# Optimization experiments

Measured on AMD Instinct MI355X. Metric: run time of the kernel, lower is better.

The kernel has to match this reference:

```python
import jax, jax.numpy as jnp
import numpy as np

B, C, N, D, H, NC = 128, 9, 2048, 192, 384, 18  # batch, in_chans, time, embed, mlp_hidden, classes


def setup_inputs() -> dict:
    key = jax.random.key(0)
    ks = jax.random.split(key, 18)
    rn = lambda k, sh, s=0.02: jax.random.normal(k, sh, dtype=jnp.float32) * s
    return {
        "x": jax.random.normal(ks[0], (B, C, N), dtype=jnp.float32),
        "conv_w": rn(ks[1], (D, C, 3)),
        "conv_b": jnp.zeros((D,), jnp.float32),
        "pos_embed": jnp.zeros((1, N, D), jnp.float32),
        "qkv_w": rn(ks[2], (3 * D, D)),
        "qkv_b": jnp.zeros((3 * D,), jnp.float32),
        "proj_w": rn(ks[3], (D, D)),
        "proj_b": jnp.zeros((D,), jnp.float32),
        "ln1_g": jnp.ones((D,), jnp.float32),
        "ln1_b": jnp.zeros((D,), jnp.float32),
        "mlp_w1": rn(ks[4], (H, D)),
        "mlp_b1": jnp.zeros((H,), jnp.float32),
        "mlp_w2": rn(ks[5], (D, H)),
        "mlp_b2": jnp.zeros((D,), jnp.float32),
        "ln2_g": jnp.ones((D,), jnp.float32),
        "ln2_b": jnp.zeros((D,), jnp.float32),
        "head_w": rn(ks[6], (NC, D)),
        "head_b": jnp.zeros((NC,), jnp.float32),
    }


def _ln(x, g, b, eps=1e-5):
    m = x.mean(-1, keepdims=True)
    v = ((x - m) ** 2).mean(-1, keepdims=True)
    return (x - m) * jax.lax.rsqrt(v + eps) * g + b


def reference(x, conv_w, conv_b, pos_embed, qkv_w, qkv_b, proj_w, proj_b,
              ln1_g, ln1_b, mlp_w1, mlp_b1, mlp_w2, mlp_b2, ln2_g, ln2_b,
              head_w, head_b):
    # patch embed: Conv1d(C->D, k=3, pad=1), then [B, N, D]
    h = jax.lax.conv_general_dilated(
        x, conv_w, window_strides=(1,), padding=[(1, 1)],
        dimension_numbers=("NCH", "OIH", "NCH")) + conv_b[None, :, None]
    h = jnp.transpose(h, (0, 2, 1)) + pos_embed  # [B, N, D]

    # linear (Performer-style) attention with ReLU feature maps
    hn = _ln(h, ln1_g, ln1_b)
    qkv = hn @ qkv_w.T + qkv_b  # [B, N, 3D]
    q, k, v = jnp.split(qkv, 3, axis=-1)
    q = jax.nn.relu(q)
    k = jax.nn.relu(k)
    kv = jnp.einsum("bnd,bne->bde", k, v)       # [B, D, D]
    num = jnp.einsum("bnd,bde->bne", q, kv)      # [B, N, D]
    # NOTE: original sums q over BOTH token and feature dims -> scalar per batch
    denom = q.sum(axis=(1, 2))[:, None, None]
    attn = num / (denom + 1e-6)
    h = h + attn @ proj_w.T + proj_b

    # MLP block (exact GELU, as torch nn.GELU default)
    hn2 = _ln(h, ln2_g, ln2_b)
    m = jax.nn.gelu(hn2 @ mlp_w1.T + mlp_b1, approximate=False)
    h = h + m @ mlp_w2.T + mlp_b2

    # head: AdaptiveAvgPool1d(1) over time, then Linear
    pooled = h.mean(axis=1)  # [B, D]
    return pooled @ head_w.T + head_b  # [B, NC]
```

## Files before the change

kernel.cpp:

```cpp
#include <hip/hip_runtime.h>
#include <cmath>

#define B_   128
#define C_   9
#define N_   2048
#define D_   192
#define H_   384
#define NC_  18

typedef unsigned short ushort_t;
typedef __attribute__((ext_vector_type(8))) __bf16 bf16x8;
typedef __attribute__((ext_vector_type(8))) short short8;
typedef __attribute__((ext_vector_type(16))) float f32x16;

__device__ __forceinline__ ushort_t f2bf(float x) {
    unsigned u = __float_as_uint(x);
    return (ushort_t)((u + 0x7fffu + ((u >> 16) & 1u)) >> 16);
}
__device__ __forceinline__ float bf2f(ushort_t h) {
    return __uint_as_float(((unsigned)h) << 16);
}
__device__ __forceinline__ bf16x8 ldfrag(const ushort_t* p) {
    short8 s = *(const short8*)p;
    return __builtin_bit_cast(bf16x8, s);
}

__global__ __launch_bounds__(192) void conv_ln_k(
    const float* __restrict__ x, const float* __restrict__ w,
    const float* __restrict__ cb, const float* __restrict__ pos,
    const float* __restrict__ lng, const float* __restrict__ lnb,
    float* __restrict__ h, ushort_t* __restrict__ oh, ushort_t* __restrict__ ol)
{
    const int n0 = blockIdx.x * 64;
    const int b  = blockIdx.y;
    const int d  = threadIdx.x;

    __shared__ float xs[C_][66];
    __shared__ float tile[64][193];
    __shared__ float ps[64][3], pq[64][3];
    __shared__ float mm[64], rr[64];

    for (int e = threadIdx.x; e < C_ * 66; e += 192) {
        int c = e / 66, i = e % 66;
        int n = n0 - 1 + i;
        xs[c][i] = (n >= 0 && n < N_) ? x[((size_t)b * C_ + c) * N_ + n] : 0.f;
    }
    float wr[C_][3];
#pragma unroll
    for (int c = 0; c < C_; ++c)
#pragma unroll
        for (int t = 0; t < 3; ++t) wr[c][t] = w[(d * C_ + c) * 3 + t];
    const float bias = cb[d];
    __syncthreads();

    for (int i = 0; i < 64; ++i) {
        float acc = bias + pos[(size_t)(n0 + i) * D_ + d];
#pragma unroll
        for (int c = 0; c < C_; ++c)
#pragma unroll
            for (int t = 0; t < 3; ++t) acc += xs[c][i + t] * wr[c][t];
        tile[i][d] = acc;
    }
    __syncthreads();

    {
        int row = threadIdx.x & 63, part = threadIdx.x >> 6;
        float s = 0.f, q = 0.f;
        const float* tr = &tile[row][part * 64];
#pragma unroll 8
        for (int j = 0; j < 64; ++j) { float v = tr[j]; s += v; q += v * v; }
        ps[row][part] = s; pq[row][part] = q;
    }
    __syncthreads();
    if (threadIdx.x < 64) {
        int r = threadIdx.x;
        float s = ps[r][0] + ps[r][1] + ps[r][2];
        float q = pq[r][0] + pq[r][1] + pq[r][2];
        float m = s * (1.f / D_);
        mm[r] = m;
        rr[r] = rsqrtf(q * (1.f / D_) - m * m + 1e-5f);
    }
    __syncthreads();
    {
        const float gd = lng[d], bd = lnb[d];
        for (int i = 0; i < 64; ++i) {
            float v = tile[i][d];
            size_t idx = ((size_t)b * N_ + n0 + i) * D_ + d;
            h[idx] = v;
            float nv = (v - mm[i]) * rr[i] * gd + bd;
            ushort_t hb = f2bf(nv);
            oh[idx] = hb;
            ol[idx] = f2bf(nv - bf2f(hb));
        }
    }
}

__global__ __launch_bounds__(256) void splitw_pack_k(
    const float* __restrict__ w, ushort_t* __restrict__ hi, ushort_t* __restrict__ lo,
    int NW, int K)
{
    int i = blockIdx.x * 256 + threadIdx.x;
    if (i >= NW * K) return;
    int row = i / K, k = i % K;
    int g = row / 192, c = row % 192;
    float v = w[i];
    ushort_t hb = f2bf(v);
    size_t o = (size_t)g * K * 192 + (size_t)(k >> 4) * 3072 + (size_t)c * 16 + (k & 15);
    hi[o] = hb;
    lo[o] = f2bf(v - bf2f(hb));
}

template <int EPI, int KT, int NBY>
__global__ __launch_bounds__(256) void mgemm(
    const ushort_t* __restrict__ Ah, const ushort_t* __restrict__ Al,
    const ushort_t* __restrict__ Wh, const ushort_t* __restrict__ Wl,
    const float* __restrict__ bias, float* __restrict__ dsum,
    const float* __restrict__ lng, const float* __restrict__ lnb,
    ushort_t* __restrict__ oh, ushort_t* __restrict__ ol,
    ushort_t* __restrict__ kTh, ushort_t* __restrict__ kTl,
    ushort_t* __restrict__ vTh, ushort_t* __restrict__ vTl,
    float* __restrict__ facc)
{
    extern __shared__ ushort_t smem[];
    constexpr int NS  = KT / 16;
    constexpr int APL = 12288;

    const int tid  = threadIdx.x;
    const int lane = tid & 63;
    const int l5   = lane >> 5;
    const int wid  = tid >> 6;
    const int wr = wid >> 1, wc = wid & 1;

    int bx, by;
    {
        int gmx = gridDim.x / NBY;
        int xx = blockIdx.x & 7, ii = blockIdx.x >> 3;
        by = ii % NBY;
        bx = xx * (gmx >> 3) + ii / NBY;
    }
    const int m0 = bx * 64;
    const int batch = m0 >> 11;

    size_t wbase = 0;
    if (EPI == 0 || EPI == 1) wbase = (size_t)by * 192 * KT;
    else if (EPI == 3) wbase = (size_t)batch * D_ * D_;
    const ushort_t* Whp = Wh + wbase;
    const ushort_t* Wlp = Wl + wbase;

    auto stageChunk = [&](int kr) {
#pragma unroll
        for (int i = 0; i < 12; ++i) {
            int c = wid + i * 4;
            int plane = c & 1, k8 = c >> 1;
            const ushort_t* ap = plane ? Al : Ah;
            const ushort_t* src = ap + (size_t)(m0 + lane) * KT + kr * 192 + k8 * 8;
            __builtin_amdgcn_global_load_lds(
                (const __attribute__((address_space(1))) void*)src,
                (__attribute__((address_space(3))) void*)(smem + plane * APL + k8 * 512),
                16, 0, 0);
        }
    };

    const int wcol = (wc * 96 + (lane & 31)) * 16 + l5 * 8;
    auto loadW = [&](int sg, bf16x8* w) {
#pragma unroll
        for (int tn = 0; tn < 3; ++tn) {
            size_t off = (size_t)sg * 3072 + wcol + tn * 512;
            w[tn * 2 + 0] = ldfrag(Whp + off);
            w[tn * 2 + 1] = ldfrag(Wlp + off);
        }
    };

    f32x16 acc[3] = {};
    const int arow = (wr * 32 + (lane & 31)) * 8;

    bf16x8 w0[6], w1[6], w2[6];
    loadW(0, w0);
    if (NS > 1) loadW(1, w1);
    if (NS > 2) loadW(2, w2);

#pragma unroll
    for (int s = 0; s < NS; ++s) {
        if ((s % 12) == 0) {
            if (s) __syncthreads();
            stageChunk(s / 12);
            __syncthreads();
        }
        bf16x8* wcur = (s % 3 == 0) ? w0 : ((s % 3 == 1) ? w1 : w2);
        int ao = ((s % 12) * 2 + l5) * 512 + arow;
        bf16x8 ah = ldfrag(smem + ao);
        bf16x8 al = ldfrag(smem + APL + ao);
#pragma unroll
        for (int tn = 0; tn < 3; ++tn) {
            acc[tn] = __builtin_amdgcn_mfma_f32_32x32x16_bf16(ah, wcur[tn * 2 + 0], acc[tn], 0, 0, 0);
            acc[tn] = __builtin_amdgcn_mfma_f32_32x32x16_bf16(ah, wcur[tn * 2 + 1], acc[tn], 0, 0, 0);
            acc[tn] = __builtin_amdgcn_mfma_f32_32x32x16_bf16(al, wcur[tn * 2 + 0], acc[tn], 0, 0, 0);
        }
        if (s + 3 < NS) loadW(s + 3, wcur);
    }

    const int cb = wc * 96 + (lane & 31);
    const int rb0 = m0 + wr * 32 + 4 * l5;
    const int rl0 = wr * 32 + 4 * l5;

    if (EPI == 0) {
        if (by == 0) {
            float qsum = 0.f;
#pragma unroll
            for (int tn = 0; tn < 3; ++tn) {
                const int col = cb + tn * 32;
                const float bv = bias[col];
#pragma unroll
                for (int r = 0; r < 16; ++r) {
                    int row = rb0 + (r & 3) + 8 * (r >> 2);
                    float v = fmaxf(acc[tn][r] + bv, 0.f);
                    qsum += v;
                    ushort_t hb = f2bf(v);
                    oh[(size_t)row * D_ + col] = hb;
                    ol[(size_t)row * D_ + col] = f2bf(v - bf2f(hb));
                }
            }
            __syncthreads();
            float* red = (float*)smem;
            red[tid] = qsum;
            __syncthreads();
            for (int o = 128; o > 0; o >>= 1) {
                if (tid < o) red[tid] += red[tid + o];
                __syncthreads();
            }
            if (tid == 0) dsum[batch * 32 + ((m0 >> 6) & 31)] = red[0];
        } else {
            ushort_t* dsth = (by == 1) ? kTh : vTh;
            ushort_t* dstl = (by == 1) ? kTl : vTl;
            constexpr int STR = 72;
#pragma unroll
            for (int plane = 0; plane < 2; ++plane) {
                __syncthreads();
#pragma unroll
                for (int tn = 0; tn < 3; ++tn) {
                    const int col = cb + tn * 32;
                    const float bv = bias[by * 192 + col];
#pragma unroll
                    for (int r = 0; r < 16; ++r) {
                        int rowl = rl0 + (r & 3) + 8 * (r >> 2);
                        float v = acc[tn][r] + bv;
                        if (by == 1) v = fmaxf(v, 0.f);
                        ushort_t hb = f2bf(v);
                        smem[col * STR + rowl] = plane ? f2bf(v - bf2f(hb)) : hb;
                    }
                }
                __syncthreads();
                if (tid < 192) {
                    ushort_t* dst = plane ? dstl : dsth;
                    size_t gbase = ((size_t)batch * 192 + tid) * (size_t)N_ + (m0 & 2047);
#pragma unroll
                    for (int i2 = 0; i2 < 8; ++i2)
                        *(uint4*)(dst + gbase + i2 * 8) = *(const uint4*)&smem[tid * STR + i2 * 8];
                }
            }
        }
    } else if (EPI == 1) {
#pragma unroll
        for (int tn = 0; tn < 3; ++tn) {
            const int colg = by * 192 + cb + tn * 32;
            const float bv = bias[colg];
#pragma unroll
            for (int r = 0; r < 16; ++r) {
                int row = rb0 + (r & 3) + 8 * (r >> 2);
                float v = acc[tn][r] + bv;
                float gv = 0.5f * v * (1.f + erff(v * 0.70710678118654752f));
                ushort_t hb = f2bf(gv);
                oh[(size_t)row * H_ + colg] = hb;
                ol[(size_t)row * H_ + colg] = f2bf(gv - bf2f(hb));
            }
        }
    } else if (EPI == 2) {
        float tsum[3] = {0.f, 0.f, 0.f};
#pragma unroll
        for (int tn = 0; tn < 3; ++tn) {
            const int col = cb + tn * 32;
            const float bv = bias[col];
#pragma unroll
            for (int r = 0; r < 16; ++r) {
                int row = rb0 + (r & 3) + 8 * (r >> 2);
                float v = facc[(size_t)row * D_ + col] + acc[tn][r] + bv;
                facc[(size_t)row * D_ + col] = v;
                tsum[tn] += v;
            }
        }
#pragma unroll
        for (int tn = 0; tn < 3; ++tn) {
            float t = tsum[tn];
            t += __shfl_xor(t, 32);
            if (l5 == 0) atomicAdd(&dsum[(size_t)batch * D_ + cb + tn * 32], t);
        }
    } else if (EPI == 3) {
        float ds = 0.f;
        const float* dp = dsum + batch * 32;
#pragma unroll
        for (int j = 0; j < 32; ++j) ds += dp[j];
        const float s = 1.f / (ds + 1e-6f);
#pragma unroll
        for (int tn = 0; tn < 3; ++tn) {
            const int col = cb + tn * 32;
            const float bv = bias[col];
#pragma unroll
            for (int r = 0; r < 16; ++r) {
                int row = rb0 + (r & 3) + 8 * (r >> 2);
                float v = facc[(size_t)row * D_ + col] + acc[tn][r] * s + bv;
                facc[(size_t)row * D_ + col] = v;
                acc[tn][r] = v;
            }
        }
        __syncthreads();
        float* ls = (float*)smem;
        float* lq = ls + 128;
        float* lm = lq + 128;
        float* lr = lm + 64;
#pragma unroll
        for (int r = 0; r < 16; ++r) {
            float pv = acc[0][r] + acc[1][r] + acc[2][r];
            float qv = acc[0][r] * acc[0][r] + acc[1][r] * acc[1][r] + acc[2][r] * acc[2][r];
#pragma unroll
            for (int off = 1; off <= 16; off <<= 1) {
                pv += __shfl_xor(pv, off);
                qv += __shfl_xor(qv, off);
            }
            if ((lane & 31) == 0) {
                int rl = rl0 + (r & 3) + 8 * (r >> 2);
                ls[rl * 2 + wc] = pv;
                lq[rl * 2 + wc] = qv;
            }
        }
        __syncthreads();
        if (tid < 64) {
            float sv = ls[tid * 2] + ls[tid * 2 + 1];
            float qv = lq[tid * 2] + lq[tid * 2 + 1];
            float mv = sv * (1.f / D_);
            lm[tid] = mv;
            lr[tid] = rsqrtf(qv * (1.f / D_) - mv * mv + 1e-5f);
        }
        __syncthreads();
#pragma unroll
        for (int tn = 0; tn < 3; ++tn) {
            const int col = cb + tn * 32;
            const float gv = lng[col], bv2 = lnb[col];
#pragma unroll
            for (int r = 0; r < 16; ++r) {
                int rl = rl0 + (r & 3) + 8 * (r >> 2);
                float nv = (acc[tn][r] - lm[rl]) * lr[rl] * gv + bv2;
                ushort_t hb = f2bf(nv);
                size_t idx = (size_t)(m0 + rl) * D_ + col;
                oh[idx] = hb;
                ol[idx] = f2bf(nv - bf2f(hb));
            }
        }
    }
}

__global__ __launch_bounds__(256) void mgemm_kv(
    const ushort_t* __restrict__ Ah, const ushort_t* __restrict__ Al,
    const ushort_t* __restrict__ Wh, const ushort_t* __restrict__ Wl,
    float* __restrict__ facc, size_t span)
{
    extern __shared__ ushort_t smem[];
    constexpr int BM = 64;
    constexpr int APL = BM * 32, AK = BM * 8, AELEMS = BM * 64;
    constexpr int BUFE = AELEMS + 12288;
    constexpr int ACH = 8, NCH = ACH + 24;

    const int tid  = threadIdx.x;
    const int lane = tid & 63;
    const int l5   = lane >> 5;
    const int wid  = tid >> 6;
    const int wr = wid >> 1, wc = wid & 1;
    const int bx = blockIdx.x;
    const int m0 = bx * BM;

    const size_t wbase = (size_t)(bx / 3) * 192 * (size_t)N_;
    const ushort_t* Whp = Wh + wbase;
    const ushort_t* Wlp = Wl + wbase;

    const int seg = N_ / gridDim.z;
    const int kbeg = blockIdx.z * seg, kend = kbeg + seg;

    auto stage = [&](int buf, int k0) {
        const int base = buf * BUFE;
#pragma unroll
        for (int i = 0; i < NCH / 4; ++i) {
            int c = wid + i * 4;
            const ushort_t* src;
            int dst;
            if (c < ACH) {
                int koct = c & 3, tt = c >> 2;
                int plane = tt & 1;
                const ushort_t* ap = plane ? Al : Ah;
                src = ap + (size_t)(m0 + lane) * N_ + k0 + koct * 8;
                dst = plane * APL + koct * AK;
            } else {
                int c2 = c - ACH;
                int koct = c2 & 3, tt = c2 >> 2;
                int plane = tt & 1, rb = tt >> 1;
                const ushort_t* wp = plane ? Wlp : Whp;
                src = wp + (size_t)(rb * 64 + lane) * N_ + k0 + koct * 8;
                dst = AELEMS + plane * 6144 + koct * 1536 + rb * 512;
            }
            __builtin_amdgcn_global_load_lds(
                (const __attribute__((address_space(1))) void*)src,
                (__attribute__((address_space(3))) void*)(smem + base + dst),
                16, 0, 0);
        }
    };

    f32x16 acc[3] = {};

    const int nt = (kend - kbeg) / 32;
    stage(0, kbeg);
    __syncthreads();
    int cur = 0;
    for (int t = 0; t < nt; ++t) {
        if (t + 1 < nt) stage(cur ^ 1, kbeg + (t + 1) * 32);
        const ushort_t* bb = smem + cur * BUFE;
#pragma unroll
        for (int kh = 0; kh < 2; ++kh) {
            int ao = (kh * 2 + l5) * AK + (wr * 32 + (lane & 31)) * 8;
            bf16x8 ah = ldfrag(bb + ao);
            bf16x8 al = ldfrag(bb + APL + ao);
#pragma unroll
            for (int tn = 0; tn < 3; ++tn) {
                int wo = AELEMS + (kh * 2 + l5) * 1536 + (wc * 96 + tn * 32 + (lane & 31)) * 8;
                bf16x8 wh = ldfrag(bb + wo);
                bf16x8 wl = ldfrag(bb + wo + 6144);
                acc[tn] = __builtin_amdgcn_mfma_f32_32x32x16_bf16(ah, wh, acc[tn], 0, 0, 0);
                acc[tn] = __builtin_amdgcn_mfma_f32_32x32x16_bf16(ah, wl, acc[tn], 0, 0, 0);
                acc[tn] = __builtin_amdgcn_mfma_f32_32x32x16_bf16(al, wh, acc[tn], 0, 0, 0);
            }
        }
        __syncthreads();
        cur ^= 1;
    }

    float* fz = facc + (size_t)blockIdx.z * span;
    const int cb = wc * 96 + (lane & 31);
    const int rb0 = m0 + wr * 32 + 4 * l5;
#pragma unroll
    for (int tn = 0; tn < 3; ++tn) {
        const int col = cb + tn * 32;
#pragma unroll
        for (int r = 0; r < 16; ++r) {
            int row = rb0 + (r & 3) + 8 * (r >> 2);
            fz[(size_t)row * D_ + col] = acc[tn][r];
        }
    }
}

__global__ __launch_bounds__(256) void kv2_k(
    const float* __restrict__ pw, const float* __restrict__ kvs, size_t span,
    ushort_t* __restrict__ oh, ushort_t* __restrict__ ol)
{
    __shared__ float As[16][68];
    __shared__ float Ws[16][68];
    const int tid = threadIdx.x;
    const int tx = tid & 15, ty = tid >> 4;
    const int m0 = blockIdx.x * 64;
    const int n0 = blockIdx.y * 64;
    const int b = blockIdx.z;
    const int lm = tid >> 2;
    const int lk = (tid & 3) * 4;

    float acc[4][4] = {};
    for (int k0 = 0; k0 < D_; k0 += 16) {
        float4 av = *(const float4*)(pw + (size_t)(m0 + lm) * D_ + k0 + lk);
        As[lk + 0][lm] = av.x; As[lk + 1][lm] = av.y;
        As[lk + 2][lm] = av.z; As[lk + 3][lm] = av.w;
        const float* base = kvs + (size_t)b * D_ * D_ + (size_t)(n0 + lm) * D_ + k0 + lk;
        float4 wv = {0.f, 0.f, 0.f, 0.f};
#pragma unroll
        for (int z = 0; z < 8; ++z) {
            float4 t = *(const float4*)(base + z * span);
            wv.x += t.x; wv.y += t.y; wv.z += t.z; wv.w += t.w;
        }
        Ws[lk + 0][lm] = wv.x; Ws[lk + 1][lm] = wv.y;
        Ws[lk + 2][lm] = wv.z; Ws[lk + 3][lm] = wv.w;
        __syncthreads();
#pragma unroll
        for (int kk = 0; kk < 16; ++kk) {
            float4 a4 = *(const float4*)&As[kk][ty * 4];
            float4 w4 = *(const float4*)&Ws[kk][tx * 4];
            float a[4] = {a4.x, a4.y, a4.z, a4.w};
            float w[4] = {w4.x, w4.y, w4.z, w4.w};
#pragma unroll
            for (int i = 0; i < 4; ++i)
#pragma unroll
                for (int j = 0; j < 4; ++j) acc[i][j] += a[i] * w[j];
        }
        __syncthreads();
    }
    const int d0 = n0 + tx * 4;
#pragma unroll
    for (int i = 0; i < 4; ++i) {
        ushort_t hb[4], lb[4];
#pragma unroll
        for (int j = 0; j < 4; ++j) {
            float v = acc[i][j];
            hb[j] = f2bf(v);
            lb[j] = f2bf(v - bf2f(hb[j]));
        }
        const int e = m0 + ty * 4 + i;
        size_t off = (size_t)b * D_ * D_ + ((size_t)(d0 >> 4) * 192 + e) * 16 + (d0 & 15);
        *(uint2*)&oh[off] = make_uint2((unsigned)hb[0] | ((unsigned)hb[1] << 16),
                                       (unsigned)hb[2] | ((unsigned)hb[3] << 16));
        *(uint2*)&ol[off] = make_uint2((unsigned)lb[0] | ((unsigned)lb[1] << 16),
                                       (unsigned)lb[2] | ((unsigned)lb[3] << 16));
    }
}

__global__ __launch_bounds__(192) void head_k(
    const float* __restrict__ pooled, const float* __restrict__ hw,
    const float* __restrict__ hb, float* __restrict__ out)
{
    const int b = blockIdx.x, d = threadIdx.x;
    __shared__ float p[D_];
    p[d] = pooled[(size_t)b * D_ + d] * (1.f / N_);
    __syncthreads();
    if (d < NC_) {
        float acc = hb[d];
        for (int e = 0; e < D_; ++e) acc += p[e] * hw[d * D_ + e];
        out[b * NC_ + d] = acc;
    }
}

extern "C" void kernel_launch(void* const* d_in, const int* in_sizes, int n_in,
                              void* d_out, int out_size, void* d_ws, size_t ws_size,
                              hipStream_t stream) {
    (void)in_sizes; (void)n_in; (void)out_size;

    const float* x      = (const float*)d_in[0];
    const float* conv_w = (const float*)d_in[1];
    const float* conv_b = (const float*)d_in[2];
    const float* pos    = (const float*)d_in[3];
    const float* qkv_w  = (const float*)d_in[4];
    const float* qkv_b  = (const float*)d_in[5];
    const float* proj_w = (const float*)d_in[6];
    const float* proj_b = (const float*)d_in[7];
    const float* ln1_g  = (const float*)d_in[8];
    const float* ln1_b  = (const float*)d_in[9];
    const float* mlp_w1 = (const float*)d_in[10];
    const float* mlp_b1 = (const float*)d_in[11];
    const float* mlp_w2 = (const float*)d_in[12];
    const float* mlp_b2 = (const float*)d_in[13];
    const float* ln2_g  = (const float*)d_in[14];
    const float* ln2_b  = (const float*)d_in[15];
    const float* head_w = (const float*)d_in[16];
    const float* head_b = (const float*)d_in[17];
    float* out = (float*)d_out;

    const size_t perB =
        (size_t)N_ * D_ * 4 +
        (size_t)N_ * D_ * 2 * 2 +
        (size_t)N_ * D_ * 2 * 2 +
        (size_t)N_ * D_ * 2 * 4 +
        (size_t)D_ * D_ * 2 * 2 +
        16384;
    const size_t fixedW = 2ull * (576 * 192 + 384 * 192 + 192 * 384) * 2 + 65536;
    int BC = B_;
    while (BC > 1 && fixedW + (size_t)BC * perB > ws_size) BC >>= 1;
    const int nchunks = B_ / BC;
    const size_t rows = (size_t)BC * N_;

    char* p = (char*)d_ws;
    auto alloc = [&](size_t bytes) -> char* {
        char* r = p;
        p += (bytes + 255) & ~(size_t)255;
        return r;
    };
    ushort_t* qw_hi = (ushort_t*)alloc(576 * 192 * 2);
    ushort_t* qw_lo = (ushort_t*)alloc(576 * 192 * 2);
    ushort_t* w1_hi = (ushort_t*)alloc(384 * 192 * 2);
    ushort_t* w1_lo = (ushort_t*)alloc(384 * 192 * 2);
    ushort_t* w2_hi = (ushort_t*)alloc(192 * 384 * 2);
    ushort_t* w2_lo = (ushort_t*)alloc(192 * 384 * 2);

    const size_t szPl = rows * D_ * 2;
    float*    h      = (float*)alloc(rows * D_ * 4);
    ushort_t* hn_hi  = (ushort_t*)alloc(szPl);
    ushort_t* hn_lo  = (ushort_t*)alloc(szPl);
    ushort_t* q_hi   = (ushort_t*)alloc(szPl);
    ushort_t* q_lo   = (ushort_t*)alloc(szPl);
    ushort_t* kT_hi  = (ushort_t*)alloc(szPl);
    ushort_t* kT_lo  = (ushort_t*)alloc(szPl);
    ushort_t* vT_hi  = (ushort_t*)alloc(szPl);
    ushort_t* vT_lo  = (ushort_t*)alloc(szPl);
    ushort_t* kv2t_h = (ushort_t*)alloc((size_t)BC * D_ * D_ * 2);
    ushort_t* kv2t_l = (ushort_t*)alloc((size_t)BC * D_ * D_ * 2);
    float*    dsum   = (float*)alloc((size_t)BC * 32 * 4);
    float*    pooled = (float*)alloc((size_t)BC * D_ * 4);
    ushort_t* m_hi   = kT_hi;
    ushort_t* m_lo   = vT_hi;
    float*    kvs    = (float*)hn_hi;
    const size_t kvspan = (size_t)BC * D_ * D_;

    splitw_pack_k<<<(576 * 192 + 255) / 256, 256, 0, stream>>>(qkv_w, qw_hi, qw_lo, 576, 192);
    splitw_pack_k<<<(384 * 192 + 255) / 256, 256, 0, stream>>>(mlp_w1, w1_hi, w1_lo, 384, 192);
    splitw_pack_k<<<(192 * 384 + 255) / 256, 256, 0, stream>>>(mlp_w2, w2_hi, w2_lo, 192, 384);

    const int gm = (int)(rows / 64);
    const size_t SHA = 49152;
    const size_t SH4 = (size_t)(64 * 64 + 12288) * 2 * 2;

    for (int ch = 0; ch < nchunks; ++ch) {
        const int b0 = ch * BC;
        const float* xc = x + (size_t)b0 * C_ * N_;

        hipMemsetAsync(pooled, 0, (size_t)BC * D_ * 4, stream);

        conv_ln_k<<<dim3(N_ / 64, BC), 192, 0, stream>>>(
            xc, conv_w, conv_b, pos, ln1_g, ln1_b, h, hn_hi, hn_lo);
        mgemm<0, 192, 3><<<gm * 3, 256, SHA, stream>>>(
            hn_hi, hn_lo, qw_hi, qw_lo, qkv_b, dsum, nullptr, nullptr,
            q_hi, q_lo, kT_hi, kT_lo, vT_hi, vT_lo, nullptr);
        mgemm_kv<<<dim3(BC * 3, 1, 8), 256, SH4, stream>>>(
            kT_hi, kT_lo, vT_hi, vT_lo, kvs, kvspan);
        kv2_k<<<dim3(3, 3, BC), 256, 0, stream>>>(proj_w, kvs, kvspan, kv2t_h, kv2t_l);
        mgemm<3, 192, 1><<<gm, 256, SHA, stream>>>(
            q_hi, q_lo, kv2t_h, kv2t_l, proj_b, dsum, ln2_g, ln2_b,
            hn_hi, hn_lo, nullptr, nullptr, nullptr, nullptr, h);
        mgemm<1, 192, 2><<<gm * 2, 256, SHA, stream>>>(
            hn_hi, hn_lo, w1_hi, w1_lo, mlp_b1, nullptr, nullptr, nullptr,
            m_hi, m_lo, nullptr, nullptr, nullptr, nullptr, nullptr);
        mgemm<2, 384, 1><<<gm, 256, SHA, stream>>>(
            m_hi, m_lo, w2_hi, w2_lo, mlp_b2, pooled, nullptr, nullptr,
            nullptr, nullptr, nullptr, nullptr, nullptr, nullptr, h);
        head_k<<<BC, 192, 0, stream>>>(pooled, head_w, head_b, out + (size_t)b0 * NC_);
    }
}
```

Before: 1.575 ms.

## Fuse MLP up/down GEMMs into one kernel and stage epilogue stores via LDS

```diff
diff --git a/kernel.cpp b/kernel.cpp
--- a/kernel.cpp
+++ b/kernel.cpp
@@ -142,7 +142,7 @@
     const int batch = m0 >> 11;
 
     size_t wbase = 0;
-    if (EPI == 0 || EPI == 1) wbase = (size_t)by * 192 * KT;
+    if (EPI == 0) wbase = (size_t)by * 192 * KT;
     else if (EPI == 3) wbase = (size_t)batch * D_ * D_;
     const ushort_t* Whp = Wh + wbase;
     const ushort_t* Wlp = Wl + wbase;
@@ -206,22 +206,32 @@
     if (EPI == 0) {
         if (by == 0) {
             float qsum = 0.f;
+            __syncthreads();
 #pragma unroll
             for (int tn = 0; tn < 3; ++tn) {
                 const int col = cb + tn * 32;
                 const float bv = bias[col];
 #pragma unroll
                 for (int r = 0; r < 16; ++r) {
-                    int row = rb0 + (r & 3) + 8 * (r >> 2);
+                    int rowl = rl0 + (r & 3) + 8 * (r >> 2);
                     float v = fmaxf(acc[tn][r] + bv, 0.f);
                     qsum += v;
                     ushort_t hb = f2bf(v);
-                    oh[(size_t)row * D_ + col] = hb;
-                    ol[(size_t)row * D_ + col] = f2bf(v - bf2f(hb));
+                    smem[rowl * 192 + col] = hb;
+                    smem[APL + rowl * 192 + col] = f2bf(v - bf2f(hb));
                 }
             }
             __syncthreads();
-            float* red = (float*)smem;
+            {
+                size_t gb = (size_t)m0 * 192;
+#pragma unroll
+                for (int j = 0; j < 6; ++j) {
+                    int idx = (tid * 6 + j) * 8;
+                    *(uint4*)(oh + gb + idx) = *(const uint4*)&smem[idx];
+                    *(uint4*)(ol + gb + idx) = *(const uint4*)&smem[APL + idx];
+                }
+            }
+            float* red = (float*)(smem + 2 * APL);
             red[tid] = qsum;
             __syncthreads();
             for (int o = 128; o > 0; o >>= 1) {
@@ -259,41 +269,6 @@
                 }
             }
         }
-    } else if (EPI == 1) {
-#pragma unroll
-        for (int tn = 0; tn < 3; ++tn) {
-            const int colg = by * 192 + cb + tn * 32;
-            const float bv = bias[colg];
-#pragma unroll
-            for (int r = 0; r < 16; ++r) {
-                int row = rb0 + (r & 3) + 8 * (r >> 2);
-                float v = acc[tn][r] + bv;
-                float gv = 0.5f * v * (1.f + erff(v * 0.70710678118654752f));
-                ushort_t hb = f2bf(gv);
-                oh[(size_t)row * H_ + colg] = hb;
-                ol[(size_t)row * H_ + colg] = f2bf(gv - bf2f(hb));
-            }
-        }
-    } else if (EPI == 2) {
-        float tsum[3] = {0.f, 0.f, 0.f};
-#pragma unroll
-        for (int tn = 0; tn < 3; ++tn) {
-            const int col = cb + tn * 32;
-            const float bv = bias[col];
-#pragma unroll
-            for (int r = 0; r < 16; ++r) {
-                int row = rb0 + (r & 3) + 8 * (r >> 2);
-                float v = facc[(size_t)row * D_ + col] + acc[tn][r] + bv;
-                facc[(size_t)row * D_ + col] = v;
-                tsum[tn] += v;
-            }
-        }
-#pragma unroll
-        for (int tn = 0; tn < 3; ++tn) {
-            float t = tsum[tn];
-            t += __shfl_xor(t, 32);
-            if (l5 == 0) atomicAdd(&dsum[(size_t)batch * D_ + cb + tn * 32], t);
-        }
     } else if (EPI == 3) {
         float ds = 0.f;
         const float* dp = dsum + batch * 32;
@@ -313,7 +288,7 @@
             }
         }
         __syncthreads();
-        float* ls = (float*)smem;
+        float* ls = (float*)(smem + 2 * APL);
         float* lq = ls + 128;
         float* lm = lq + 128;
         float* lr = lm + 64;
@@ -350,11 +325,154 @@
                 int rl = rl0 + (r & 3) + 8 * (r >> 2);
                 float nv = (acc[tn][r] - lm[rl]) * lr[rl] * gv + bv2;
                 ushort_t hb = f2bf(nv);
-                size_t idx = (size_t)(m0 + rl) * D_ + col;
-                oh[idx] = hb;
-                ol[idx] = f2bf(nv - bf2f(hb));
-            }
-        }
+                smem[rl * 192 + col] = hb;
+                smem[APL + rl * 192 + col] = f2bf(nv - bf2f(hb));
+            }
+        }
+        __syncthreads();
+        {
+            size_t gb = (size_t)m0 * 192;
+#pragma unroll
+            for (int j = 0; j < 6; ++j) {
+                int idx = (tid * 6 + j) * 8;
+                *(uint4*)(oh + gb + idx) = *(const uint4*)&smem[idx];
+                *(uint4*)(ol + gb + idx) = *(const uint4*)&smem[APL + idx];
+            }
+        }
+    }
+}
+
+__global__ __launch_bounds__(256) void fused_mlp(
+    const ushort_t* __restrict__ Ah, const ushort_t* __restrict__ Al,
+    const ushort_t* __restrict__ W1h, const ushort_t* __restrict__ W1l,
+    const ushort_t* __restrict__ W2h, const ushort_t* __restrict__ W2l,
+    const float* __restrict__ b1, const float* __restrict__ b2,
+    float* __restrict__ h, float* __restrict__ pooled)
+{
+    extern __shared__ ushort_t smem[];
+    constexpr int APL = 12288;
+
+    const int tid  = threadIdx.x;
+    const int lane = tid & 63;
+    const int l5   = lane >> 5;
+    const int wid  = tid >> 6;
+    const int wr = wid >> 1, wc = wid & 1;
+
+    int bx;
+    { int xx = blockIdx.x & 7, ii = blockIdx.x >> 3; bx = xx * (gridDim.x >> 3) + ii; }
+    const int m0 = bx * 64;
+    const int batch = m0 >> 11;
+
+#pragma unroll
+    for (int i = 0; i < 12; ++i) {
+        int c = wid + i * 4;
+        int plane = c & 1, k8 = c >> 1;
+        const ushort_t* ap = plane ? Al : Ah;
+        const ushort_t* src = ap + (size_t)(m0 + lane) * 192 + k8 * 8;
+        __builtin_amdgcn_global_load_lds(
+            (const __attribute__((address_space(1))) void*)src,
+            (__attribute__((address_space(3))) void*)(smem + plane * APL + k8 * 512),
+            16, 0, 0);
+    }
+    __syncthreads();
+
+    const int wcol = (wc * 96 + (lane & 31)) * 16 + l5 * 8;
+    const int arow = (wr * 32 + (lane & 31)) * 8;
+
+    auto loadWf = [&](const ushort_t* Wh, const ushort_t* Wl, int sg, bf16x8* w) {
+#pragma unroll
+        for (int tn = 0; tn < 3; ++tn) {
+            size_t off = (size_t)sg * 3072 + wcol + tn * 512;
+            w[tn * 2 + 0] = ldfrag(Wh + off);
+            w[tn * 2 + 1] = ldfrag(Wl + off);
+        }
+    };
+
+    f32x16 accm[2][3] = {};
+#pragma unroll
+    for (int g = 0; g < 2; ++g) {
+        const ushort_t* Wh = W1h + g * 36864;
+        const ushort_t* Wl = W1l + g * 36864;
+        bf16x8 w0[6], w1[6], w2[6];
+        loadWf(Wh, Wl, 0, w0);
+        loadWf(Wh, Wl, 1, w1);
+        loadWf(Wh, Wl, 2, w2);
+#pragma unroll
+        for (int s = 0; s < 12; ++s) {
+            bf16x8* wcur = (s % 3 == 0) ? w0 : ((s % 3 == 1) ? w1 : w2);
+            int ao = (s * 2 + l5) * 512 + arow;
+            bf16x8 ah = ldfrag(smem + ao);
+            bf16x8 al = ldfrag(smem + APL + ao);
+#pragma unroll
+            for (int tn = 0; tn < 3; ++tn) {
+                accm[g][tn] = __builtin_amdgcn_mfma_f32_32x32x16_bf16(ah, wcur[tn * 2 + 0], accm[g][tn], 0, 0, 0);
+                accm[g][tn] = __builtin_amdgcn_mfma_f32_32x32x16_bf16(ah, wcur[tn * 2 + 1], accm[g][tn], 0, 0, 0);
+                accm[g][tn] = __builtin_amdgcn_mfma_f32_32x32x16_bf16(al, wcur[tn * 2 + 0], accm[g][tn], 0, 0, 0);
+            }
+            if (s + 3 < 12) loadWf(Wh, Wl, s + 3, wcur);
+        }
+    }
+
+    f32x16 acco[3] = {};
+#pragma unroll
+    for (int g = 0; g < 2; ++g) {
+        __syncthreads();
+#pragma unroll
+        for (int tn = 0; tn < 3; ++tn) {
+            const int cl = wc * 96 + tn * 32 + (lane & 31);
+            const float bv = b1[g * 192 + cl];
+#pragma unroll
+            for (int r = 0; r < 16; ++r) {
+                int rowl = wr * 32 + 4 * l5 + (r & 3) + 8 * (r >> 2);
+                float v = accm[g][tn][r] + bv;
+                float gv = 0.5f * v * (1.f + erff(v * 0.70710678118654752f));
+                ushort_t hb = f2bf(gv);
+                int ad = ((cl >> 3) * 64 + rowl) * 8 + (cl & 7);
+                smem[ad] = hb;
+                smem[APL + ad] = f2bf(gv - bf2f(hb));
+            }
+        }
+        __syncthreads();
+        bf16x8 w0[6], w1[6], w2[6];
+        loadWf(W2h, W2l, g * 12 + 0, w0);
+        loadWf(W2h, W2l, g * 12 + 1, w1);
+        loadWf(W2h, W2l, g * 12 + 2, w2);
+#pragma unroll
+        for (int s = 0; s < 12; ++s) {
+            bf16x8* wcur = (s % 3 == 0) ? w0 : ((s % 3 == 1) ? w1 : w2);
+            int ao = (s * 2 + l5) * 512 + arow;
+            bf16x8 ah = ldfrag(smem + ao);
+            bf16x8 al = ldfrag(smem + APL + ao);
+#pragma unroll
+            for (int tn = 0; tn < 3; ++tn) {
+                acco[tn] = __builtin_amdgcn_mfma_f32_32x32x16_bf16(ah, wcur[tn * 2 + 0], acco[tn], 0, 0, 0);
+                acco[tn] = __builtin_amdgcn_mfma_f32_32x32x16_bf16(ah, wcur[tn * 2 + 1], acco[tn], 0, 0, 0);
+                acco[tn] = __builtin_amdgcn_mfma_f32_32x32x16_bf16(al, wcur[tn * 2 + 0], acco[tn], 0, 0, 0);
+            }
+            if (s + 3 < 12) loadWf(W2h, W2l, g * 12 + s + 3, wcur);
+        }
+    }
+
+    const int cb = wc * 96 + (lane & 31);
+    const int rb0 = m0 + wr * 32 + 4 * l5;
+    float tsum[3] = {0.f, 0.f, 0.f};
+#pragma unroll
+    for (int tn = 0; tn < 3; ++tn) {
+        const int col = cb + tn * 32;
+        const float bv = b2[col];
+#pragma unroll
+        for (int r = 0; r < 16; ++r) {
+            int row = rb0 + (r & 3) + 8 * (r >> 2);
+            float v = h[(size_t)row * D_ + col] + acco[tn][r] + bv;
+            h[(size_t)row * D_ + col] = v;
+            tsum[tn] += v;
+        }
+    }
+#pragma unroll
+    for (int tn = 0; tn < 3; ++tn) {
+        float t = tsum[tn];
+        t += __shfl_xor(t, 32);
+        if (l5 == 0) atomicAdd(&pooled[(size_t)batch * D_ + cb + tn * 32], t);
     }
 }
 
@@ -595,8 +713,6 @@
     ushort_t* kv2t_l = (ushort_t*)alloc((size_t)BC * D_ * D_ * 2);
     float*    dsum   = (float*)alloc((size_t)BC * 32 * 4);
     float*    pooled = (float*)alloc((size_t)BC * D_ * 4);
-    ushort_t* m_hi   = kT_hi;
-    ushort_t* m_lo   = vT_hi;
     float*    kvs    = (float*)hn_hi;
     const size_t kvspan = (size_t)BC * D_ * D_;
 
@@ -605,7 +721,8 @@
     splitw_pack_k<<<(192 * 384 + 255) / 256, 256, 0, stream>>>(mlp_w2, w2_hi, w2_lo, 192, 384);
 
     const int gm = (int)(rows / 64);
-    const size_t SHA = 49152;
+    const size_t SHL = 50688;
+    const size_t SHM = 49152;
     const size_t SH4 = (size_t)(64 * 64 + 12288) * 2 * 2;
 
     for (int ch = 0; ch < nchunks; ++ch) {
@@ -616,21 +733,17 @@
 
         conv_ln_k<<<dim3(N_ / 64, BC), 192, 0, stream>>>(
             xc, conv_w, conv_b, pos, ln1_g, ln1_b, h, hn_hi, hn_lo);
-        mgemm<0, 192, 3><<<gm * 3, 256, SHA, stream>>>(
+        mgemm<0, 192, 3><<<gm * 3, 256, SHL, stream>>>(
             hn_hi, hn_lo, qw_hi, qw_lo, qkv_b, dsum, nullptr, nullptr,
             q_hi, q_lo, kT_hi, kT_lo, vT_hi, vT_lo, nullptr);
         mgemm_kv<<<dim3(BC * 3, 1, 8), 256, SH4, stream>>>(
             kT_hi, kT_lo, vT_hi, vT_lo, kvs, kvspan);
         kv2_k<<<dim3(3, 3, BC), 256, 0, stream>>>(proj_w, kvs, kvspan, kv2t_h, kv2t_l);
-        mgemm<3, 192, 1><<<gm, 256, SHA, stream>>>(
+        mgemm<3, 192, 1><<<gm, 256, SHL, stream>>>(
             q_hi, q_lo, kv2t_h, kv2t_l, proj_b, dsum, ln2_g, ln2_b,
             hn_hi, hn_lo, nullptr, nullptr, nullptr, nullptr, h);
-        mgemm<1, 192, 2><<<gm * 2, 256, SHA, stream>>>(
-            hn_hi, hn_lo, w1_hi, w1_lo, mlp_b1, nullptr, nullptr, nullptr,
-            m_hi, m_lo, nullptr, nullptr, nullptr, nullptr, nullptr);
-        mgemm<2, 384, 1><<<gm, 256, SHA, stream>>>(
-            m_hi, m_lo, w2_hi, w2_lo, mlp_b2, pooled, nullptr, nullptr,
-            nullptr, nullptr, nullptr, nullptr, nullptr, nullptr, h);
+        fused_mlp<<<gm, 256, SHM, stream>>>(
+            hn_hi, hn_lo, w1_hi, w1_lo, w2_hi, w2_lo, mlp_b1, mlp_b2, h, pooled);
         head_k<<<BC, 192, 0, stream>>>(pooled, head_w, head_b, out + (size_t)b0 * NC_);
     }
 }
```

After: 1.557 ms. No clear change (-1.2%).
